# Optimization experiments

Measured on AMD Instinct MI355X. Metric: run time of the kernel, lower is better.

The kernel has to match this reference:

```python
import jax, jax.numpy as jnp
import numpy as np

N_HEADS = 8
D_HEAD = 64


def setup_inputs() -> dict:
    key = jax.random.key(0)
    ks = jax.random.split(key, 7)
    B, Sq, Dm = 16, 4096, 512
    Skv, Dc = 77, 768
    inner = N_HEADS * D_HEAD  # 512
    s = lambda d: 1.0 / np.sqrt(d)
    return {
        "x": jax.random.normal(ks[0], (B, Sq, Dm), jnp.float32),
        "context": jax.random.normal(ks[1], (B, Skv, Dc), jnp.float32),
        "Wq": jax.random.normal(ks[2], (Dm, inner), jnp.float32) * s(Dm),
        "Wk": jax.random.normal(ks[3], (Dc, inner), jnp.float32) * s(Dc),
        "Wv": jax.random.normal(ks[4], (Dc, inner), jnp.float32) * s(Dc),
        "Wout": jax.random.normal(ks[5], (inner, inner), jnp.float32) * s(inner),
        "bout": jnp.zeros((inner,), jnp.float32),
    }


def reference(x, context, Wq, Wk, Wv, Wout, bout):
    B, Sq, _ = x.shape
    Skv = context.shape[1]
    scale = D_HEAD ** (-0.5)
    # projections (no bias)
    q = (x @ Wq).reshape(B, Sq, N_HEADS, D_HEAD)
    k = (context @ Wk).reshape(B, Skv, N_HEADS, D_HEAD)
    v = (context @ Wv).reshape(B, Skv, N_HEADS, D_HEAD)
    # scores: [B, H, Sq, Skv]
    score = jnp.einsum("bqhd,bkhd->bhqk", q, k) * scale
    weights = jax.nn.softmax(score, axis=-1)
    attn = jnp.einsum("bhqk,bkhd->bqhd", weights, v)
    h = attn.reshape(B, Sq, N_HEADS * D_HEAD)
    return h @ Wout + bout
```

## Files before the change

### kernel.cpp

```cpp
#include <hip/hip_runtime.h>


typedef unsigned short u16;
typedef unsigned int u32;
typedef _Float16 f16;
typedef __attribute__((ext_vector_type(8))) _Float16 half8;
typedef __attribute__((ext_vector_type(4))) _Float16 half4;
typedef __attribute__((ext_vector_type(4))) float f32x4;

__device__ __forceinline__ f32x4 mfma16h(half8 a, half8 b, f32x4 c) {
    return __builtin_amdgcn_mfma_f32_16x16x32_f16(a, b, c, 0, 0, 0);
}
__device__ __forceinline__ void gl_lds16(const f16* g, f16* l) {
    __builtin_amdgcn_global_load_lds(
        (const __attribute__((address_space(1))) void*)g,
        (__attribute__((address_space(3))) void*)l, 16, 0, 0);
}

__global__ __launch_bounds__(256) void prep(
    const float* __restrict__ Wq, const float* __restrict__ Wk,
    const float* __restrict__ Wv, const float* __restrict__ Wo,
    f16* __restrict__ WqT, f16* __restrict__ WkT,
    f16* __restrict__ WvT, f16* __restrict__ WoT,
    f16* __restrict__ vT, f16* __restrict__ kbuf)
{
    int idx = blockIdx.x * 256 + threadIdx.x;
    if (idx < 1310720) {
        const float* W; f16* T; int K; int base;
        if (idx < 262144)        { W = Wq; T = WqT; K = 512; base = 0; }
        else if (idx < 655360)   { W = Wk; T = WkT; K = 768; base = 262144; }
        else if (idx < 1048576)  { W = Wv; T = WvT; K = 768; base = 655360; }
        else                     { W = Wo; T = WoT; K = 512; base = 1048576; }
        int j = idx - base;
        int n = j / K, k = j - n * K;
        T[j] = (f16)W[(size_t)k * 512 + n];
        return;
    }
    int i = idx - 1310720;
    const int nv = 16 * 512 * 19;
    if (i < nv) {
        int g = i / 19, s = i - g * 19;
        vT[(size_t)g * 96 + 77 + s] = (f16)0.f;
    } else {
        int j = i - nv;
        if (j < 8 * 512) kbuf[(size_t)1232 * 512 + j] = (f16)0.f;
    }
}

__global__ __launch_bounds__(256) void gemm_kv(
    const float* __restrict__ A, const f16* __restrict__ Bt,
    f16* __restrict__ kbuf, f16* __restrict__ vT)
{
    __shared__ f16 lA[64 * 40];
    __shared__ f16 lB[64 * 40];

    const int t = threadIdx.x;
    const int lane = t & 63;
    const int w = t >> 6;
    const int wr = w >> 1, wc = w & 1;
    const int m0 = blockIdx.x * 64, n0 = blockIdx.y * 64;
    const int ar = lane & 15;
    const int kc = (lane >> 4) << 3;

    const int srow = t >> 2;
    const int sc8  = (t & 3) << 3;

    f32x4 acc[2][2] = {};

    for (int k0 = 0; k0 < 768; k0 += 32) {
        float4 v0 = make_float4(0.f, 0.f, 0.f, 0.f);
        float4 v1 = make_float4(0.f, 0.f, 0.f, 0.f);
        int gr = m0 + srow;
        if (gr < 1232) {
            v0 = *(const float4*)(A + (size_t)gr * 768 + k0 + sc8);
            v1 = *(const float4*)(A + (size_t)gr * 768 + k0 + sc8 + 4);
        }
        half8 ha = {(f16)v0.x, (f16)v0.y, (f16)v0.z, (f16)v0.w,
                    (f16)v1.x, (f16)v1.y, (f16)v1.z, (f16)v1.w};
        *(half8*)(lA + srow * 40 + sc8) = ha;
        *(half8*)(lB + srow * 40 + sc8) =
            *(const half8*)(Bt + (size_t)(n0 + srow) * 768 + k0 + sc8);
        __syncthreads();

        half8 fa[2], fb[2];
        #pragma unroll
        for (int m = 0; m < 2; ++m)
            fa[m] = *(const half8*)(lA + (wr * 32 + m * 16 + ar) * 40 + kc);
        #pragma unroll
        for (int n = 0; n < 2; ++n)
            fb[n] = *(const half8*)(lB + (wc * 32 + n * 16 + ar) * 40 + kc);
        #pragma unroll
        for (int m = 0; m < 2; ++m)
            #pragma unroll
            for (int n = 0; n < 2; ++n)
                acc[m][n] = mfma16h(fa[m], fb[n], acc[m][n]);
        __syncthreads();
    }

    #pragma unroll
    for (int n = 0; n < 2; ++n) {
        int col = n0 + wc * 32 + n * 16 + ar;
        #pragma unroll
        for (int m = 0; m < 2; ++m) {
            #pragma unroll
            for (int r = 0; r < 4; ++r) {
                int row = m0 + wr * 32 + m * 16 + ((lane >> 4) << 2) + r;
                if (row < 1232) {
                    f16 v = (f16)acc[m][n][r];
                    if (col < 512) {
                        kbuf[(size_t)row * 512 + col] = v;
                    } else {
                        int bb = row / 77;
                        int si = row - bb * 77;
                        vT[((size_t)bb * 512 + (col - 512)) * 96 + si] = v;
                    }
                }
            }
        }
    }
}

__global__ __launch_bounds__(256, 2) void gemm_x16(
    const float* __restrict__ A, const f16* __restrict__ B,
    f16* __restrict__ CHalf, int M, int N, int K)
{
    __shared__ f16 sA[2][128 * 32];
    __shared__ f16 sB[2][256 * 32];

    const int t = threadIdx.x;
    const int lane = t & 63;
    const int w = t >> 6;
    const int wr = w >> 1, wc = w & 1;

    const int f = blockIdx.x + gridDim.x * blockIdx.y;
    const int cpx = (gridDim.x * gridDim.y) >> 3;
    const int logical = (f & 7) * cpx + (f >> 3);
    const int m0 = (logical / gridDim.x) * 128;
    const int n0 = (logical % gridDim.x) * 256;

    const int ar = lane & 15;
    const int kc = (lane >> 4) << 3;

    const int arow = t >> 3;
    const int acol = (t & 7) << 2;
    const int brow = lane >> 2;
    const int bcol = (lane & 3) << 3;

    f32x4 acc[4][8] = {};
    f32x4 rA[4];

    auto LOAD_A = [&](int kt) {
        #pragma unroll
        for (int j = 0; j < 4; ++j)
            rA[j] = *(const f32x4*)(A + (size_t)(m0 + arow + j * 32) * K
                                      + (kt << 5) + acol);
    };
    auto WRITE_A = [&](int buf) {
        #pragma unroll
        for (int j = 0; j < 4; ++j) {
            half4 h = {(f16)rA[j].x, (f16)rA[j].y, (f16)rA[j].z, (f16)rA[j].w};
            *(half4*)(&sA[buf][(arow + j * 32) * 32 + acol]) = h;
        }
    };
    auto STAGE_B = [&](int buf, int kt) {
        #pragma unroll
        for (int j = 0; j < 4; ++j) {
            const int ci = w * 4 + j;
            gl_lds16(B + (size_t)(n0 + ci * 16 + brow) * K + (kt << 5) + bcol,
                     &sB[buf][ci * 512]);
        }
    };

    const int nk = K >> 5;
    LOAD_A(0);
    STAGE_B(0, 0);
    WRITE_A(0);
    __syncthreads();

    int cur = 0;
    for (int kt = 0; kt < nk; ++kt) {
        if (kt + 1 < nk) {
            LOAD_A(kt + 1);
            STAGE_B(cur ^ 1, kt + 1);
        }

        half8 fa[4], fb[8];
        #pragma unroll
        for (int m = 0; m < 4; ++m)
            fa[m] = *(const half8*)(&sA[cur][(wr * 64 + m * 16 + ar) * 32 + kc]);
        #pragma unroll
        for (int n = 0; n < 8; ++n)
            fb[n] = *(const half8*)(&sB[cur][(wc * 128 + n * 16 + ar) * 32 + kc]);

        __builtin_amdgcn_s_setprio(1);
        #pragma unroll
        for (int m = 0; m < 4; ++m)
            #pragma unroll
            for (int n = 0; n < 8; ++n)
                acc[m][n] = mfma16h(fa[m], fb[n], acc[m][n]);
        __builtin_amdgcn_s_setprio(0);

        if (kt + 1 < nk) WRITE_A(cur ^ 1);
        __syncthreads();
        cur ^= 1;
    }

    #pragma unroll
    for (int n = 0; n < 8; ++n) {
        int col = n0 + wc * 128 + n * 16 + ar;
        #pragma unroll
        for (int m = 0; m < 4; ++m) {
            #pragma unroll
            for (int r = 0; r < 4; ++r) {
                int row = m0 + wr * 64 + m * 16 + ((lane >> 4) << 2) + r;
                CHalf[(size_t)row * N + col] = (f16)acc[m][n][r];
            }
        }
    }
}

__global__ __launch_bounds__(256, 2) void gemm_h16(
    const f16* __restrict__ A, const f16* __restrict__ B,
    const float* __restrict__ bias, float* __restrict__ C,
    int M, int N, int K)
{
    __shared__ f16 sA[2][128 * 32];
    __shared__ f16 sB[2][256 * 32];

    const int t = threadIdx.x;
    const int lane = t & 63;
    const int w = t >> 6;
    const int wr = w >> 1, wc = w & 1;

    const int f = blockIdx.x + gridDim.x * blockIdx.y;
    const int cpx = (gridDim.x * gridDim.y) >> 3;
    const int logical = (f & 7) * cpx + (f >> 3);
    const int m0 = (logical / gridDim.x) * 128;
    const int n0 = (logical % gridDim.x) * 256;

    const int ar = lane & 15;
    const int kc = (lane >> 4) << 3;
    const int srow = lane >> 2;
    const int scol = (lane & 3) << 3;

    f32x4 acc[4][8] = {};

    auto STAGE = [&](int buf, int kt) {
        #pragma unroll
        for (int j = 0; j < 2; ++j) {
            const int ci = w * 2 + j;
            gl_lds16(A + (size_t)(m0 + ci * 16 + srow) * K + (kt << 5) + scol,
                     &sA[buf][ci * 512]);
        }
        #pragma unroll
        for (int j = 0; j < 4; ++j) {
            const int ci = w * 4 + j;
            gl_lds16(B + (size_t)(n0 + ci * 16 + srow) * K + (kt << 5) + scol,
                     &sB[buf][ci * 512]);
        }
    };

    const int nk = K >> 5;
    STAGE(0, 0);
    __syncthreads();

    int cur = 0;
    for (int kt = 0; kt < nk; ++kt) {
        if (kt + 1 < nk) STAGE(cur ^ 1, kt + 1);

        half8 fa[4], fb[8];
        #pragma unroll
        for (int m = 0; m < 4; ++m)
            fa[m] = *(const half8*)(&sA[cur][(wr * 64 + m * 16 + ar) * 32 + kc]);
        #pragma unroll
        for (int n = 0; n < 8; ++n)
            fb[n] = *(const half8*)(&sB[cur][(wc * 128 + n * 16 + ar) * 32 + kc]);

        __builtin_amdgcn_s_setprio(1);
        #pragma unroll
        for (int m = 0; m < 4; ++m)
            #pragma unroll
            for (int n = 0; n < 8; ++n)
                acc[m][n] = mfma16h(fa[m], fb[n], acc[m][n]);
        __builtin_amdgcn_s_setprio(0);
        __syncthreads();
        cur ^= 1;
    }

    #pragma unroll
    for (int n = 0; n < 8; ++n) {
        int col = n0 + wc * 128 + n * 16 + ar;
        float bv = bias[col];
        #pragma unroll
        for (int m = 0; m < 4; ++m) {
            #pragma unroll
            for (int r = 0; r < 4; ++r) {
                int row = m0 + wr * 64 + m * 16 + ((lane >> 4) << 2) + r;
                C[(size_t)row * N + col] = acc[m][n][r] + bv;
            }
        }
    }
}

__global__ __launch_bounds__(256) void attn_h16(
    const f16* __restrict__ q, const f16* __restrict__ k,
    const f16* __restrict__ vT, f16* __restrict__ outA)
{
    constexpr int PST = 104;
    __shared__ f16 sP[4 * 32 * PST];

    const int t = threadIdx.x;
    const int lane = t & 63;
    const int w = t >> 6;
    const int ar = lane & 15;
    const int kg = lane >> 4;
    const int kc = kg << 3;
    const int b = blockIdx.z, head = blockIdx.y;
    const size_t qrow0 = (size_t)b * 4096 + blockIdx.x * 128 + w * 32;

    f32x4 accs[2][5] = {};
    #pragma unroll
    for (int ks = 0; ks < 2; ++ks) {
        const int d = head * 64 + ks * 32 + kc;
        half8 ah[2];
        #pragma unroll
        for (int m = 0; m < 2; ++m)
            ah[m] = *(const half8*)(q + (qrow0 + m * 16 + ar) * 512 + d);
        #pragma unroll
        for (int n = 0; n < 5; ++n) {
            half8 bh = *(const half8*)(k + ((size_t)(b * 77 + n * 16 + ar)) * 512 + d);
            #pragma unroll
            for (int m = 0; m < 2; ++m)
                accs[m][n] = mfma16h(ah[m], bh, accs[m][n]);
        }
    }

    #pragma unroll
    for (int m = 0; m < 2; ++m) {
        #pragma unroll
        for (int r = 0; r < 4; ++r) {
            float mx = -1e30f;
            #pragma unroll
            for (int n = 0; n < 5; ++n) {
                float v = accs[m][n][r] * 0.125f;
                if (n == 4 && ar >= 13) v = -1e30f;
                accs[m][n][r] = v;
                mx = fmaxf(mx, v);
            }
            mx = fmaxf(mx, __shfl_xor(mx, 1));
            mx = fmaxf(mx, __shfl_xor(mx, 2));
            mx = fmaxf(mx, __shfl_xor(mx, 4));
            mx = fmaxf(mx, __shfl_xor(mx, 8));
            float sum = 0.f;
            #pragma unroll
            for (int n = 0; n < 5; ++n) {
                float e = __expf(accs[m][n][r] - mx);
                accs[m][n][r] = e;
                sum += e;
            }
            sum += __shfl_xor(sum, 1);
            sum += __shfl_xor(sum, 2);
            sum += __shfl_xor(sum, 4);
            sum += __shfl_xor(sum, 8);
            float inv = 1.f / sum;
            #pragma unroll
            for (int n = 0; n < 5; ++n) accs[m][n][r] *= inv;
        }
    }

    f16* myP = sP + w * 32 * PST;
    for (int i = lane; i < 32 * 12; i += 64) {
        int row = i / 12, c = 80 + (i % 12) * 2;
        *(u32*)(myP + row * PST + c) = 0;
    }
    #pragma unroll
    for (int m = 0; m < 2; ++m)
        #pragma unroll
        for (int n = 0; n < 5; ++n)
            #pragma unroll
            for (int r = 0; r < 4; ++r)
                myP[(m * 16 + kg * 4 + r) * PST + n * 16 + ar] = (f16)accs[m][n][r];

    f32x4 accp[2][4] = {};
    #pragma unroll
    for (int ks = 0; ks < 3; ++ks) {
        half8 pa[2];
        #pragma unroll
        for (int m = 0; m < 2; ++m)
            pa[m] = *(const half8*)(myP + (m * 16 + ar) * PST + ks * 32 + kc);
        #pragma unroll
        for (int n = 0; n < 4; ++n) {
            half8 bh = *(const half8*)(vT + ((size_t)b * 512 + head * 64 + n * 16 + ar) * 96 + ks * 32 + kc);
            #pragma unroll
            for (int m = 0; m < 2; ++m)
                accp[m][n] = mfma16h(pa[m], bh, accp[m][n]);
        }
    }

    #pragma unroll
    for (int m = 0; m < 2; ++m)
        #pragma unroll
        for (int n = 0; n < 4; ++n)
            #pragma unroll
            for (int r = 0; r < 4; ++r)
                outA[(qrow0 + m * 16 + kg * 4 + r) * 512 + head * 64 + n * 16 + ar]
                    = (f16)accp[m][n][r];
}

extern "C" void kernel_launch(void* const* d_in, const int* in_sizes, int n_in,
                              void* d_out, int out_size, void* d_ws, size_t ws_size,
                              hipStream_t stream)
{
    const float* x    = (const float*)d_in[0];
    const float* ctx  = (const float*)d_in[1];
    const float* Wq   = (const float*)d_in[2];
    const float* Wk   = (const float*)d_in[3];
    const float* Wv   = (const float*)d_in[4];
    const float* Wout = (const float*)d_in[5];
    const float* bout = (const float*)d_in[6];

    char* ws = (char*)d_ws;
    size_t off = 0;
    auto alloc = [&](size_t bytes) -> void* {
        void* p = ws + off;
        off += (bytes + 255) & ~(size_t)255;
        return p;
    };
    f16* WqT = (f16*)alloc(512 * 512 * 2);
    f16* WkT = (f16*)alloc(768 * 512 * 2);
    f16* WvT = (f16*)alloc(768 * 512 * 2);
    f16* WoT = (f16*)alloc(512 * 512 * 2);
    f16* kbuf = (f16*)alloc((size_t)1240 * 512 * 2);
    f16* vT   = (f16*)alloc((size_t)16 * 512 * 96 * 2);
    f16* qh   = (f16*)alloc((size_t)65536 * 512 * 2);
    f16* attnA = (f16*)alloc((size_t)65536 * 512 * 2);
    (void)ws_size; (void)in_sizes; (void)n_in; (void)out_size;

    prep<<<dim3(5744), dim3(256), 0, stream>>>(
        Wq, Wk, Wv, Wout, WqT, WkT, WvT, WoT, vT, kbuf);

    gemm_kv<<<dim3(20, 16), dim3(256), 0, stream>>>(ctx, WkT, kbuf, vT);

    gemm_x16<<<dim3(2, 512), dim3(256), 0, stream>>>(
        x, WqT, qh, 65536, 512, 512);

    attn_h16<<<dim3(32, 8, 16), dim3(256), 0, stream>>>(qh, kbuf, vT, attnA);

    gemm_h16<<<dim3(2, 512), dim3(256), 0, stream>>>(
        attnA, WoT, bout, (float*)d_out, 65536, 512, 512);
}
```

Before: 215.1 us.

## Fuse Q projection GEMM with cross-attention into one kernel

Replaces the separate Q-projection GEMM and attention kernels with one kernel. Each block computes a 128x128 Q tile (two heads), stages it in LDS, then runs QK^T, softmax and PV per 16-row slice straight from that tile. This removes the fp16 Q buffer's round trip through global memory and one kernel launch. In exchange the N tile shrinks from 256 to 128, so the fp32 x input is read four times instead of twice. The min-blocks hint is dropped from the launch bounds, and the attention phase now runs serially per warp after the GEMM.

```diff
diff --git a/kernel.cpp b/kernel.cpp
--- a/kernel.cpp
+++ b/kernel.cpp
@@ -120,12 +120,12 @@
     }
 }
 
-__global__ __launch_bounds__(256, 2) void gemm_x16(
+__global__ __launch_bounds__(256) void qattn16(
     const float* __restrict__ A, const f16* __restrict__ B,
-    f16* __restrict__ CHalf, int M, int N, int K)
+    const f16* __restrict__ kbuf, const f16* __restrict__ vT,
+    f16* __restrict__ attnA)
 {
-    __shared__ f16 sA[2][128 * 32];
-    __shared__ f16 sB[2][256 * 32];
+    __shared__ f16 smem[25088];
 
     const int t = threadIdx.x;
     const int lane = t & 63;
@@ -136,86 +136,161 @@
     const int cpx = (gridDim.x * gridDim.y) >> 3;
     const int logical = (f & 7) * cpx + (f >> 3);
     const int m0 = (logical / gridDim.x) * 128;
-    const int n0 = (logical % gridDim.x) * 256;
+    const int n0 = (logical % gridDim.x) * 128;
 
     const int ar = lane & 15;
-    const int kc = (lane >> 4) << 3;
+    const int kg = lane >> 4;
+    const int kc = kg << 3;
 
     const int arow = t >> 3;
     const int acol = (t & 7) << 2;
     const int brow = lane >> 2;
     const int bcol = (lane & 3) << 3;
 
-    f32x4 acc[4][8] = {};
+    f16* sA0 = smem;
+    f16* sB0 = smem + 8192;
+
+    f32x4 acc[4][4] = {};
     f32x4 rA[4];
 
     auto LOAD_A = [&](int kt) {
         #pragma unroll
         for (int j = 0; j < 4; ++j)
-            rA[j] = *(const f32x4*)(A + (size_t)(m0 + arow + j * 32) * K
+            rA[j] = *(const f32x4*)(A + (size_t)(m0 + arow + j * 32) * 512
                                       + (kt << 5) + acol);
     };
     auto WRITE_A = [&](int buf) {
         #pragma unroll
         for (int j = 0; j < 4; ++j) {
             half4 h = {(f16)rA[j].x, (f16)rA[j].y, (f16)rA[j].z, (f16)rA[j].w};
-            *(half4*)(&sA[buf][(arow + j * 32) * 32 + acol]) = h;
+            *(half4*)(sA0 + buf * 4096 + (arow + j * 32) * 32 + acol) = h;
         }
     };
     auto STAGE_B = [&](int buf, int kt) {
         #pragma unroll
-        for (int j = 0; j < 4; ++j) {
-            const int ci = w * 4 + j;
-            gl_lds16(B + (size_t)(n0 + ci * 16 + brow) * K + (kt << 5) + bcol,
-                     &sB[buf][ci * 512]);
+        for (int j = 0; j < 2; ++j) {
+            const int ci = w * 2 + j;
+            gl_lds16(B + (size_t)(n0 + ci * 16 + brow) * 512 + (kt << 5) + bcol,
+                     sB0 + buf * 4096 + ci * 512);
         }
     };
 
-    const int nk = K >> 5;
     LOAD_A(0);
     STAGE_B(0, 0);
     WRITE_A(0);
     __syncthreads();
 
     int cur = 0;
-    for (int kt = 0; kt < nk; ++kt) {
-        if (kt + 1 < nk) {
+    for (int kt = 0; kt < 16; ++kt) {
+        if (kt + 1 < 16) {
             LOAD_A(kt + 1);
             STAGE_B(cur ^ 1, kt + 1);
         }
 
-        half8 fa[4], fb[8];
+        half8 fa[4], fb[4];
         #pragma unroll
         for (int m = 0; m < 4; ++m)
-            fa[m] = *(const half8*)(&sA[cur][(wr * 64 + m * 16 + ar) * 32 + kc]);
-        #pragma unroll
-        for (int n = 0; n < 8; ++n)
-            fb[n] = *(const half8*)(&sB[cur][(wc * 128 + n * 16 + ar) * 32 + kc]);
+            fa[m] = *(const half8*)(sA0 + cur * 4096 + (wr * 64 + m * 16 + ar) * 32 + kc);
+        #pragma unroll
+        for (int n = 0; n < 4; ++n)
+            fb[n] = *(const half8*)(sB0 + cur * 4096 + (wc * 64 + n * 16 + ar) * 32 + kc);
 
         __builtin_amdgcn_s_setprio(1);
         #pragma unroll
         for (int m = 0; m < 4; ++m)
             #pragma unroll
-            for (int n = 0; n < 8; ++n)
+            for (int n = 0; n < 4; ++n)
                 acc[m][n] = mfma16h(fa[m], fb[n], acc[m][n]);
         __builtin_amdgcn_s_setprio(0);
 
-        if (kt + 1 < nk) WRITE_A(cur ^ 1);
+        if (kt + 1 < 16) WRITE_A(cur ^ 1);
         __syncthreads();
         cur ^= 1;
     }
 
+    f16* qt  = smem + w * 4608;
+    f16* myP = smem + 18432 + w * 1664;
+    const int head = (n0 >> 6) + wc;
+    const int gr0 = m0 + wr * 64;
+    const int b = gr0 >> 12;
+
     #pragma unroll
-    for (int n = 0; n < 8; ++n) {
-        int col = n0 + wc * 128 + n * 16 + ar;
-        #pragma unroll
-        for (int m = 0; m < 4; ++m) {
-            #pragma unroll
-            for (int r = 0; r < 4; ++r) {
-                int row = m0 + wr * 64 + m * 16 + ((lane >> 4) << 2) + r;
-                CHalf[(size_t)row * N + col] = (f16)acc[m][n][r];
-            }
-        }
+    for (int m = 0; m < 4; ++m)
+        #pragma unroll
+        for (int n = 0; n < 4; ++n)
+            #pragma unroll
+            for (int r = 0; r < 4; ++r)
+                qt[(m * 16 + kg * 4 + r) * 72 + n * 16 + ar] = (f16)acc[m][n][r];
+
+    for (int i = lane; i < 16 * 12; i += 64) {
+        int row = i / 12, c = 80 + (i % 12) * 2;
+        *(u32*)(myP + row * 104 + c) = 0;
+    }
+
+    #pragma unroll 1
+    for (int q4 = 0; q4 < 4; ++q4) {
+        f32x4 accs[5] = {};
+        #pragma unroll
+        for (int ks = 0; ks < 2; ++ks) {
+            half8 ah = *(const half8*)(qt + (q4 * 16 + ar) * 72 + ks * 32 + kc);
+            #pragma unroll
+            for (int n = 0; n < 5; ++n) {
+                half8 bh = *(const half8*)(kbuf + (size_t)(b * 77 + n * 16 + ar) * 512
+                                                + head * 64 + ks * 32 + kc);
+                accs[n] = mfma16h(ah, bh, accs[n]);
+            }
+        }
+        #pragma unroll
+        for (int r = 0; r < 4; ++r) {
+            float mx = -1e30f;
+            #pragma unroll
+            for (int n = 0; n < 5; ++n) {
+                float v = accs[n][r] * 0.125f;
+                if (n == 4 && ar >= 13) v = -1e30f;
+                accs[n][r] = v;
+                mx = fmaxf(mx, v);
+            }
+            mx = fmaxf(mx, __shfl_xor(mx, 1));
+            mx = fmaxf(mx, __shfl_xor(mx, 2));
+            mx = fmaxf(mx, __shfl_xor(mx, 4));
+            mx = fmaxf(mx, __shfl_xor(mx, 8));
+            float sum = 0.f;
+            #pragma unroll
+            for (int n = 0; n < 5; ++n) {
+                float e = __expf(accs[n][r] - mx);
+                accs[n][r] = e;
+                sum += e;
+            }
+            sum += __shfl_xor(sum, 1);
+            sum += __shfl_xor(sum, 2);
+            sum += __shfl_xor(sum, 4);
+            sum += __shfl_xor(sum, 8);
+            float inv = 1.f / sum;
+            #pragma unroll
+            for (int n = 0; n < 5; ++n) accs[n][r] *= inv;
+        }
+        #pragma unroll
+        for (int n = 0; n < 5; ++n)
+            #pragma unroll
+            for (int r = 0; r < 4; ++r)
+                myP[(kg * 4 + r) * 104 + n * 16 + ar] = (f16)accs[n][r];
+        f32x4 accp[4] = {};
+        #pragma unroll
+        for (int ks = 0; ks < 3; ++ks) {
+            half8 pa = *(const half8*)(myP + ar * 104 + ks * 32 + kc);
+            #pragma unroll
+            for (int n = 0; n < 4; ++n) {
+                half8 bh = *(const half8*)(vT +
+                    ((size_t)b * 512 + head * 64 + n * 16 + ar) * 96 + ks * 32 + kc);
+                accp[n] = mfma16h(pa, bh, accp[n]);
+            }
+        }
+        #pragma unroll
+        for (int n = 0; n < 4; ++n)
+            #pragma unroll
+            for (int r = 0; r < 4; ++r)
+                attnA[(size_t)(gr0 + q4 * 16 + kg * 4 + r) * 512
+                      + head * 64 + n * 16 + ar] = (f16)accp[n][r];
     }
 }
 
@@ -300,111 +375,6 @@
             }
         }
     }
-}
-
-__global__ __launch_bounds__(256) void attn_h16(
-    const f16* __restrict__ q, const f16* __restrict__ k,
-    const f16* __restrict__ vT, f16* __restrict__ outA)
-{
-    constexpr int PST = 104;
-    __shared__ f16 sP[4 * 32 * PST];
-
-    const int t = threadIdx.x;
-    const int lane = t & 63;
-    const int w = t >> 6;
-    const int ar = lane & 15;
-    const int kg = lane >> 4;
-    const int kc = kg << 3;
-    const int b = blockIdx.z, head = blockIdx.y;
-    const size_t qrow0 = (size_t)b * 4096 + blockIdx.x * 128 + w * 32;
-
-    f32x4 accs[2][5] = {};
-    #pragma unroll
-    for (int ks = 0; ks < 2; ++ks) {
-        const int d = head * 64 + ks * 32 + kc;
-        half8 ah[2];
-        #pragma unroll
-        for (int m = 0; m < 2; ++m)
-            ah[m] = *(const half8*)(q + (qrow0 + m * 16 + ar) * 512 + d);
-        #pragma unroll
-        for (int n = 0; n < 5; ++n) {
-            half8 bh = *(const half8*)(k + ((size_t)(b * 77 + n * 16 + ar)) * 512 + d);
-            #pragma unroll
-            for (int m = 0; m < 2; ++m)
-                accs[m][n] = mfma16h(ah[m], bh, accs[m][n]);
-        }
-    }
-
-    #pragma unroll
-    for (int m = 0; m < 2; ++m) {
-        #pragma unroll
-        for (int r = 0; r < 4; ++r) {
-            float mx = -1e30f;
-            #pragma unroll
-            for (int n = 0; n < 5; ++n) {
-                float v = accs[m][n][r] * 0.125f;
-                if (n == 4 && ar >= 13) v = -1e30f;
-                accs[m][n][r] = v;
-                mx = fmaxf(mx, v);
-            }
-            mx = fmaxf(mx, __shfl_xor(mx, 1));
-            mx = fmaxf(mx, __shfl_xor(mx, 2));
-            mx = fmaxf(mx, __shfl_xor(mx, 4));
-            mx = fmaxf(mx, __shfl_xor(mx, 8));
-            float sum = 0.f;
-            #pragma unroll
-            for (int n = 0; n < 5; ++n) {
-                float e = __expf(accs[m][n][r] - mx);
-                accs[m][n][r] = e;
-                sum += e;
-            }
-            sum += __shfl_xor(sum, 1);
-            sum += __shfl_xor(sum, 2);
-            sum += __shfl_xor(sum, 4);
-            sum += __shfl_xor(sum, 8);
-            float inv = 1.f / sum;
-            #pragma unroll
-            for (int n = 0; n < 5; ++n) accs[m][n][r] *= inv;
-        }
-    }
-
-    f16* myP = sP + w * 32 * PST;
-    for (int i = lane; i < 32 * 12; i += 64) {
-        int row = i / 12, c = 80 + (i % 12) * 2;
-        *(u32*)(myP + row * PST + c) = 0;
-    }
-    #pragma unroll
-    for (int m = 0; m < 2; ++m)
-        #pragma unroll
-        for (int n = 0; n < 5; ++n)
-            #pragma unroll
-            for (int r = 0; r < 4; ++r)
-                myP[(m * 16 + kg * 4 + r) * PST + n * 16 + ar] = (f16)accs[m][n][r];
-
-    f32x4 accp[2][4] = {};
-    #pragma unroll
-    for (int ks = 0; ks < 3; ++ks) {
-        half8 pa[2];
-        #pragma unroll
-        for (int m = 0; m < 2; ++m)
-            pa[m] = *(const half8*)(myP + (m * 16 + ar) * PST + ks * 32 + kc);
-        #pragma unroll
-        for (int n = 0; n < 4; ++n) {
-            half8 bh = *(const half8*)(vT + ((size_t)b * 512 + head * 64 + n * 16 + ar) * 96 + ks * 32 + kc);
-            #pragma unroll
-            for (int m = 0; m < 2; ++m)
-                accp[m][n] = mfma16h(pa[m], bh, accp[m][n]);
-        }
-    }
-
-    #pragma unroll
-    for (int m = 0; m < 2; ++m)
-        #pragma unroll
-        for (int n = 0; n < 4; ++n)
-            #pragma unroll
-            for (int r = 0; r < 4; ++r)
-                outA[(qrow0 + m * 16 + kg * 4 + r) * 512 + head * 64 + n * 16 + ar]
-                    = (f16)accp[m][n][r];
 }
 
 extern "C" void kernel_launch(void* const* d_in, const int* in_sizes, int n_in,
@@ -432,7 +402,6 @@
     f16* WoT = (f16*)alloc(512 * 512 * 2);
     f16* kbuf = (f16*)alloc((size_t)1240 * 512 * 2);
     f16* vT   = (f16*)alloc((size_t)16 * 512 * 96 * 2);
-    f16* qh   = (f16*)alloc((size_t)65536 * 512 * 2);
     f16* attnA = (f16*)alloc((size_t)65536 * 512 * 2);
     (void)ws_size; (void)in_sizes; (void)n_in; (void)out_size;
 
@@ -441,10 +410,8 @@
 
     gemm_kv<<<dim3(20, 16), dim3(256), 0, stream>>>(ctx, WkT, kbuf, vT);
 
-    gemm_x16<<<dim3(2, 512), dim3(256), 0, stream>>>(
-        x, WqT, qh, 65536, 512, 512);
-
-    attn_h16<<<dim3(32, 8, 16), dim3(256), 0, stream>>>(qh, kbuf, vT, attnA);
+    qattn16<<<dim3(4, 512), dim3(256), 0, stream>>>(
+        x, WqT, kbuf, vT, attnA);
 
     gemm_h16<<<dim3(2, 512), dim3(256), 0, stream>>>(
         attnA, WoT, bout, (float*)d_out, 65536, 512, 512);
```

Result: slower. 219.9 us (+2.2%).

## Fuse K/V projection GEMM into prep kernel reading fp32 weights directly

Applied to the files above, without the earlier changes.

Merges the weight-transpose prep kernel and the K/V projection GEMM into one launch. The K/V GEMM now reads Wk/Wv directly from fp32, converting in registers, so the separate f16 transposed Wk/Wv copies are no longer written. It also uses a 64-wide K tile with register-prefetched double buffering in LDS. The aim is to save a kernel launch and the transposed-weight round trip through memory. The cost is strided scalar loads of the weight columns, and the GEMM blocks run alongside the elementwise prep blocks in one grid.

```diff
diff --git a/kernel.cpp b/kernel.cpp
--- a/kernel.cpp
+++ b/kernel.cpp
@@ -17,106 +17,140 @@
         (__attribute__((address_space(3))) void*)l, 16, 0, 0);
 }
 
-__global__ __launch_bounds__(256) void prep(
-    const float* __restrict__ Wq, const float* __restrict__ Wk,
-    const float* __restrict__ Wv, const float* __restrict__ Wo,
-    f16* __restrict__ WqT, f16* __restrict__ WkT,
-    f16* __restrict__ WvT, f16* __restrict__ WoT,
-    f16* __restrict__ vT, f16* __restrict__ kbuf)
+__global__ __launch_bounds__(256) void prep2(
+    const float* __restrict__ ctx, const float* __restrict__ Wk,
+    const float* __restrict__ Wv, const float* __restrict__ Wq,
+    const float* __restrict__ Wo,
+    f16* __restrict__ WqT, f16* __restrict__ WoT,
+    f16* __restrict__ kbuf, f16* __restrict__ vT)
 {
-    int idx = blockIdx.x * 256 + threadIdx.x;
-    if (idx < 1310720) {
-        const float* W; f16* T; int K; int base;
-        if (idx < 262144)        { W = Wq; T = WqT; K = 512; base = 0; }
-        else if (idx < 655360)   { W = Wk; T = WkT; K = 768; base = 262144; }
-        else if (idx < 1048576)  { W = Wv; T = WvT; K = 768; base = 655360; }
-        else                     { W = Wo; T = WoT; K = 512; base = 1048576; }
-        int j = idx - base;
-        int n = j / K, k = j - n * K;
-        T[j] = (f16)W[(size_t)k * 512 + n];
+    __shared__ f16 lA[2][64 * 72];
+    __shared__ f16 lB[2][64 * 72];
+
+    const int bid = blockIdx.x;
+    const int t = threadIdx.x;
+
+    if (bid < 320) {
+        const int lane = t & 63;
+        const int w = t >> 6;
+        const int ar = lane & 15;
+        const int kc = (lane >> 4) << 3;
+        const int wr = w >> 1, wc = w & 1;
+        const int m0 = (bid % 20) * 64, n0 = (bid / 20) * 64;
+
+        const float* Wsel = (n0 < 512) ? Wk : Wv;
+        const int srow = t >> 2;
+        const int sc   = (t & 3) << 4;
+        const int ncol = (n0 & 511) + srow;
+
+        f32x4 acc[2][2] = {};
+        f32x4 rA[4];
+        float rBv[16];
+
+        auto LOAD_KV = [&](int kt) {
+            const int gr = m0 + srow;
+            if (gr < 1232) {
+                const float* pa = ctx + (size_t)gr * 768 + (kt << 6) + sc;
+                #pragma unroll
+                for (int j = 0; j < 4; ++j) rA[j] = *(const f32x4*)(pa + j * 4);
+            } else {
+                #pragma unroll
+                for (int j = 0; j < 4; ++j) rA[j] = (f32x4){0.f, 0.f, 0.f, 0.f};
+            }
+            const float* pw = Wsel + (size_t)((kt << 6) + sc) * 512 + ncol;
+            #pragma unroll
+            for (int j = 0; j < 16; ++j) rBv[j] = pw[(size_t)j * 512];
+        };
+        auto WRITE_KV = [&](int buf) {
+            half8 h0 = { (f16)rA[0].x, (f16)rA[0].y, (f16)rA[0].z, (f16)rA[0].w,
+                         (f16)rA[1].x, (f16)rA[1].y, (f16)rA[1].z, (f16)rA[1].w };
+            half8 h1 = { (f16)rA[2].x, (f16)rA[2].y, (f16)rA[2].z, (f16)rA[2].w,
+                         (f16)rA[3].x, (f16)rA[3].y, (f16)rA[3].z, (f16)rA[3].w };
+            *(half8*)(&lA[buf][srow * 72 + sc])     = h0;
+            *(half8*)(&lA[buf][srow * 72 + sc + 8]) = h1;
+            half8 b0 = { (f16)rBv[0], (f16)rBv[1], (f16)rBv[2], (f16)rBv[3],
+                         (f16)rBv[4], (f16)rBv[5], (f16)rBv[6], (f16)rBv[7] };
+            half8 b1 = { (f16)rBv[8],  (f16)rBv[9],  (f16)rBv[10], (f16)rBv[11],
+                         (f16)rBv[12], (f16)rBv[13], (f16)rBv[14], (f16)rBv[15] };
+            *(half8*)(&lB[buf][srow * 72 + sc])     = b0;
+            *(half8*)(&lB[buf][srow * 72 + sc + 8]) = b1;
+        };
+
+        LOAD_KV(0);
+        WRITE_KV(0);
+        __syncthreads();
+
+        int cur = 0;
+        for (int kt = 0; kt < 12; ++kt) {
+            if (kt + 1 < 12) LOAD_KV(kt + 1);
+
+            #pragma unroll
+            for (int ks = 0; ks < 2; ++ks) {
+                half8 fa[2], fb[2];
+                #pragma unroll
+                for (int m = 0; m < 2; ++m)
+                    fa[m] = *(const half8*)(&lA[cur][(wr * 32 + m * 16 + ar) * 72
+                                                     + ks * 32 + kc]);
+                #pragma unroll
+                for (int n = 0; n < 2; ++n)
+                    fb[n] = *(const half8*)(&lB[cur][(wc * 32 + n * 16 + ar) * 72
+                                                     + ks * 32 + kc]);
+                #pragma unroll
+                for (int m = 0; m < 2; ++m)
+                    #pragma unroll
+                    for (int n = 0; n < 2; ++n)
+                        acc[m][n] = mfma16h(fa[m], fb[n], acc[m][n]);
+            }
+
+            if (kt + 1 < 12) WRITE_KV(cur ^ 1);
+            __syncthreads();
+            cur ^= 1;
+        }
+
+        #pragma unroll
+        for (int n = 0; n < 2; ++n) {
+            int col = n0 + wc * 32 + n * 16 + ar;
+            #pragma unroll
+            for (int m = 0; m < 2; ++m) {
+                #pragma unroll
+                for (int r = 0; r < 4; ++r) {
+                    int row = m0 + wr * 32 + m * 16 + ((lane >> 4) << 2) + r;
+                    if (row < 1232) {
+                        f16 v = (f16)acc[m][n][r];
+                        if (col < 512) {
+                            kbuf[(size_t)row * 512 + col] = v;
+                        } else {
+                            int bb = row / 77;
+                            int si = row - bb * 77;
+                            vT[((size_t)bb * 512 + (col - 512)) * 96 + si] = v;
+                        }
+                    }
+                }
+            }
+        }
         return;
     }
-    int i = idx - 1310720;
+
+    int idx = (bid - 320) * 256 + t;
+    if (idx < 262144) {
+        int n = idx / 512, k = idx - n * 512;
+        WqT[idx] = (f16)Wq[(size_t)k * 512 + n];
+        return;
+    }
+    idx -= 262144;
+    if (idx < 262144) {
+        int n = idx / 512, k = idx - n * 512;
+        WoT[idx] = (f16)Wo[(size_t)k * 512 + n];
+        return;
+    }
+    idx -= 262144;
     const int nv = 16 * 512 * 19;
-    if (i < nv) {
-        int g = i / 19, s = i - g * 19;
+    if (idx < nv) {
+        int g = idx / 19, s = idx - g * 19;
         vT[(size_t)g * 96 + 77 + s] = (f16)0.f;
     } else {
-        int j = i - nv;
+        int j = idx - nv;
         if (j < 8 * 512) kbuf[(size_t)1232 * 512 + j] = (f16)0.f;
-    }
-}
-
-__global__ __launch_bounds__(256) void gemm_kv(
-    const float* __restrict__ A, const f16* __restrict__ Bt,
-    f16* __restrict__ kbuf, f16* __restrict__ vT)
-{
-    __shared__ f16 lA[64 * 40];
-    __shared__ f16 lB[64 * 40];
-
-    const int t = threadIdx.x;
-    const int lane = t & 63;
-    const int w = t >> 6;
-    const int wr = w >> 1, wc = w & 1;
-    const int m0 = blockIdx.x * 64, n0 = blockIdx.y * 64;
-    const int ar = lane & 15;
-    const int kc = (lane >> 4) << 3;
-
-    const int srow = t >> 2;
-    const int sc8  = (t & 3) << 3;
-
-    f32x4 acc[2][2] = {};
-
-    for (int k0 = 0; k0 < 768; k0 += 32) {
-        float4 v0 = make_float4(0.f, 0.f, 0.f, 0.f);
-        float4 v1 = make_float4(0.f, 0.f, 0.f, 0.f);
-        int gr = m0 + srow;
-        if (gr < 1232) {
-            v0 = *(const float4*)(A + (size_t)gr * 768 + k0 + sc8);
-            v1 = *(const float4*)(A + (size_t)gr * 768 + k0 + sc8 + 4);
-        }
-        half8 ha = {(f16)v0.x, (f16)v0.y, (f16)v0.z, (f16)v0.w,
-                    (f16)v1.x, (f16)v1.y, (f16)v1.z, (f16)v1.w};
-        *(half8*)(lA + srow * 40 + sc8) = ha;
-        *(half8*)(lB + srow * 40 + sc8) =
-            *(const half8*)(Bt + (size_t)(n0 + srow) * 768 + k0 + sc8);
-        __syncthreads();
-
-        half8 fa[2], fb[2];
-        #pragma unroll
-        for (int m = 0; m < 2; ++m)
-            fa[m] = *(const half8*)(lA + (wr * 32 + m * 16 + ar) * 40 + kc);
-        #pragma unroll
-        for (int n = 0; n < 2; ++n)
-            fb[n] = *(const half8*)(lB + (wc * 32 + n * 16 + ar) * 40 + kc);
-        #pragma unroll
-        for (int m = 0; m < 2; ++m)
-            #pragma unroll
-            for (int n = 0; n < 2; ++n)
-                acc[m][n] = mfma16h(fa[m], fb[n], acc[m][n]);
-        __syncthreads();
-    }
-
-    #pragma unroll
-    for (int n = 0; n < 2; ++n) {
-        int col = n0 + wc * 32 + n * 16 + ar;
-        #pragma unroll
-        for (int m = 0; m < 2; ++m) {
-            #pragma unroll
-            for (int r = 0; r < 4; ++r) {
-                int row = m0 + wr * 32 + m * 16 + ((lane >> 4) << 2) + r;
-                if (row < 1232) {
-                    f16 v = (f16)acc[m][n][r];
-                    if (col < 512) {
-                        kbuf[(size_t)row * 512 + col] = v;
-                    } else {
-                        int bb = row / 77;
-                        int si = row - bb * 77;
-                        vT[((size_t)bb * 512 + (col - 512)) * 96 + si] = v;
-                    }
-                }
-            }
-        }
     }
 }
 
@@ -427,8 +461,6 @@
         return p;
     };
     f16* WqT = (f16*)alloc(512 * 512 * 2);
-    f16* WkT = (f16*)alloc(768 * 512 * 2);
-    f16* WvT = (f16*)alloc(768 * 512 * 2);
     f16* WoT = (f16*)alloc(512 * 512 * 2);
     f16* kbuf = (f16*)alloc((size_t)1240 * 512 * 2);
     f16* vT   = (f16*)alloc((size_t)16 * 512 * 96 * 2);
@@ -436,10 +468,8 @@
     f16* attnA = (f16*)alloc((size_t)65536 * 512 * 2);
     (void)ws_size; (void)in_sizes; (void)n_in; (void)out_size;
 
-    prep<<<dim3(5744), dim3(256), 0, stream>>>(
-        Wq, Wk, Wv, Wout, WqT, WkT, WvT, WoT, vT, kbuf);
-
-    gemm_kv<<<dim3(20, 16), dim3(256), 0, stream>>>(ctx, WkT, kbuf, vT);
+    prep2<<<dim3(2992), dim3(256), 0, stream>>>(
+        ctx, Wk, Wv, Wq, Wout, WqT, WoT, kbuf, vT);
 
     gemm_x16<<<dim3(2, 512), dim3(256), 0, stream>>>(
         x, WqT, qh, 65536, 512, 512);
```

Result: faster. 205.5 us (-4.4%).
